# Optimization experiments

Measured on AMD Instinct MI355X. Metric: run time of the kernel, lower is better.

Reference implementation:

```python
import jax, jax.numpy as jnp
import numpy as np

N_NODES = 50000
N_EDGES = 800000
NODE_DIM = 32
EDGE_DIM = 16
HID = 64
MSG_HID = 128
NUM_GRAPHS = 512
NUM_MP = 3
S2S_STEPS = 6


def _lin(k, fan_in, fan_out):
    # torch Linear default init: U(-1/sqrt(fan_in), 1/sqrt(fan_in))
    bound = 1.0 / np.sqrt(fan_in)
    kw, kb = jax.random.split(k)
    W = jax.random.uniform(kw, (fan_in, fan_out), jnp.float32, -bound, bound)
    b = jax.random.uniform(kb, (fan_out,), jnp.float32, -bound, bound)
    return W, b


def setup_inputs() -> dict:
    key = jax.random.key(0)
    ks = jax.random.split(key, 16)
    x_feat = jax.random.normal(ks[0], (N_NODES, NODE_DIM), jnp.float32)
    edge_index = jax.random.randint(ks[1], (2, N_EDGES), 0, N_NODES)
    edge_attr = jax.random.normal(ks[2], (N_EDGES, EDGE_DIM), jnp.float32)
    batch = jnp.sort(jax.random.randint(ks[3], (N_NODES,), 0, NUM_GRAPHS))
    W_emb, b_emb = _lin(ks[4], NODE_DIM, HID)
    W_m1, b_m1 = _lin(ks[5], 2 * HID + EDGE_DIM, MSG_HID)
    W_m2, b_m2 = _lin(ks[6], MSG_HID, HID)
    bnd = 1.0 / np.sqrt(HID)
    gru_W_ih = jax.random.uniform(ks[7], (3 * HID, HID), jnp.float32, -bnd, bnd)
    gru_W_hh = jax.random.uniform(ks[8], (3 * HID, HID), jnp.float32, -bnd, bnd)
    gru_b_ih = jax.random.uniform(ks[9], (3 * HID,), jnp.float32, -bnd, bnd)
    gru_b_hh = jax.random.uniform(ks[9], (3 * HID,), jnp.float32, -bnd, bnd)
    lstm_W_ih = jax.random.uniform(ks[10], (4 * HID, 2 * HID), jnp.float32, -bnd, bnd)
    lstm_W_hh = jax.random.uniform(ks[11], (4 * HID, HID), jnp.float32, -bnd, bnd)
    lstm_b_ih = jax.random.uniform(ks[12], (4 * HID,), jnp.float32, -bnd, bnd)
    lstm_b_hh = jax.random.uniform(ks[12], (4 * HID,), jnp.float32, -bnd, bnd)
    W_r1, b_r1 = _lin(ks[13], 2 * HID, HID)
    W_r2, b_r2 = _lin(ks[14], HID, 1)
    return dict(x_feat=x_feat, edge_index=edge_index, edge_attr=edge_attr, batch=batch,
                W_emb=W_emb, b_emb=b_emb, W_m1=W_m1, b_m1=b_m1, W_m2=W_m2, b_m2=b_m2,
                gru_W_ih=gru_W_ih, gru_W_hh=gru_W_hh, gru_b_ih=gru_b_ih, gru_b_hh=gru_b_hh,
                lstm_W_ih=lstm_W_ih, lstm_W_hh=lstm_W_hh, lstm_b_ih=lstm_b_ih, lstm_b_hh=lstm_b_hh,
                W_r1=W_r1, b_r1=b_r1, W_r2=W_r2, b_r2=b_r2)


def reference(x_feat, edge_index, edge_attr, batch,
              W_emb, b_emb, W_m1, b_m1, W_m2, b_m2,
              gru_W_ih, gru_W_hh, gru_b_ih, gru_b_hh,
              lstm_W_ih, lstm_W_hh, lstm_b_ih, lstm_b_hh,
              W_r1, b_r1, W_r2, b_r2):
    src, dst = edge_index[0], edge_index[1]
    x = x_feat @ W_emb + b_emb  # [N, HID]
    h = x  # GRU hidden state (seq_len=1 GRU)
    for _ in range(NUM_MP):
        # message: cat([x_i (target), x_j (source), edge_attr]) -> MLP -> scatter-add to target
        mi = jnp.concatenate([x[dst], x[src], edge_attr], axis=-1)  # [E, 2H+Ed]
        msg = jnp.maximum(mi @ W_m1 + b_m1, 0.0) @ W_m2 + b_m2  # [E, H]
        m = jax.ops.segment_sum(msg, dst, num_segments=N_NODES)  # [N, H]
        # torch GRU cell, gate order (r, z, n)
        gi = m @ gru_W_ih.T + gru_b_ih
        gh = h @ gru_W_hh.T + gru_b_hh
        ir, iz, i_n = jnp.split(gi, 3, axis=-1)
        hr, hz, h_n = jnp.split(gh, 3, axis=-1)
        r = jax.nn.sigmoid(ir + hr)
        z = jax.nn.sigmoid(iz + hz)
        n = jnp.tanh(i_n + r * h_n)
        h = (1.0 - z) * n + z * h
        x = h
    # Set2Set pooling
    qh = jnp.zeros((NUM_GRAPHS, HID), x.dtype)
    qc = jnp.zeros((NUM_GRAPHS, HID), x.dtype)
    q_star = jnp.zeros((NUM_GRAPHS, 2 * HID), x.dtype)
    for _ in range(S2S_STEPS):
        # torch LSTM cell, gate order (i, f, g, o)
        g = q_star @ lstm_W_ih.T + lstm_b_ih + qh @ lstm_W_hh.T + lstm_b_hh
        gi_, gf, gg, go = jnp.split(g, 4, axis=-1)
        qc = jax.nn.sigmoid(gf) * qc + jax.nn.sigmoid(gi_) * jnp.tanh(gg)
        qh = jax.nn.sigmoid(go) * jnp.tanh(qc)
        e = jnp.sum(x * qh[batch], axis=-1)  # [N]
        emax = jax.ops.segment_max(e, batch, num_segments=NUM_GRAPHS)
        a = jnp.exp(e - emax[batch])
        asum = jax.ops.segment_sum(a, batch, num_segments=NUM_GRAPHS)
        a = a / asum[batch]  # segment softmax
        rvec = jax.ops.segment_sum(a[:, None] * x, batch, num_segments=NUM_GRAPHS)  # [B, H]
        q_star = jnp.concatenate([qh, rvec], axis=-1)
    out = jnp.maximum(q_star @ W_r1 + b_r1, 0.0) @ W_r2 + b_r2
    return out
```

## Files before the change

kernel.cpp:

```cpp
#include <hip/hip_runtime.h>
#include <hip/hip_bf16.h>

#define HID 64
#define MSG 128
#define NDIM 32
#define EDIM 16
#define NG 512
#define SCAP 192

typedef unsigned short u16;
typedef unsigned int u32;
typedef _Float16 h8 __attribute__((ext_vector_type(8)));
typedef _Float16 h4 __attribute__((ext_vector_type(4)));
typedef _Float16 h2 __attribute__((ext_vector_type(2)));

__device__ __forceinline__ float sigm(float x){return 1.0f/(1.0f+expf(-x));}
__device__ __forceinline__ int rfl(int x){return __builtin_amdgcn_readfirstlane(x);}
__device__ __forceinline__ u32 pkh(float a, float b){
    union { h2 h; u32 u; } v; v.h[0] = (_Float16)a; v.h[1] = (_Float16)b; return v.u;
}
__device__ __forceinline__ h2 pk2h(float a, float b){
    union { __fp16 __attribute__((ext_vector_type(2))) r; h2 h; } v;
    v.r = __builtin_amdgcn_cvt_pkrtz(a, b);
    return v.h;
}
__device__ __forceinline__ float fdot2_(h2 a, u32 w, float c){
    union { u32 u; h2 h; } v; v.u = w;
    return __builtin_amdgcn_fdot2(a, v.h, c, false);
}

__global__ void k_hist(const int* __restrict__ idx, int n, int* __restrict__ cnt) {
    int i = blockIdx.x * blockDim.x + threadIdx.x;
    int stride = gridDim.x * blockDim.x;
    for (; i < n; i += stride) atomicAdd(&cnt[idx[i]], 1);
}

__global__ void k_scanA(const int* __restrict__ in, int* __restrict__ out,
                        int* __restrict__ bsum, int n) {
    __shared__ int sh[1024];
    int i = blockIdx.x * 1024 + threadIdx.x;
    int v = (i < n) ? in[i] : 0;
    sh[threadIdx.x] = v;
    __syncthreads();
    for (int off = 1; off < 1024; off <<= 1) {
        int t = (threadIdx.x >= off) ? sh[threadIdx.x - off] : 0;
        __syncthreads();
        sh[threadIdx.x] += t;
        __syncthreads();
    }
    if (i < n) out[i] = sh[threadIdx.x] - v;
    if (threadIdx.x == 1023) bsum[blockIdx.x] = sh[1023];
}
__global__ void k_scanB(const int* __restrict__ bsum, int* __restrict__ boff, int nb) {
    if (threadIdx.x == 0) {
        int r = 0;
        for (int b = 0; b < nb; b++) { boff[b] = r; r += bsum[b]; }
        boff[nb] = r;
    }
}
__global__ void k_scanC(int* __restrict__ out, const int* __restrict__ boff, int n, int nb) {
    int i = blockIdx.x * blockDim.x + threadIdx.x;
    if (i < n) out[i] += boff[i >> 10];
    else if (i == n) out[n] = boff[nb];
}

__global__ void k_gptr(const int* __restrict__ batch, int N, int* __restrict__ gptr) {
    int g = blockIdx.x * blockDim.x + threadIdx.x;
    if (g > NG) return;
    int lo = 0, hi = N;
    while (lo < hi) { int mid = (lo + hi) >> 1; if (batch[mid] < g) lo = mid + 1; else hi = mid; }
    gptr[g] = lo;
}

__global__ void k_scatter(const int* __restrict__ src, const int* __restrict__ dst, int n,
                          const int* __restrict__ ptr, int* __restrict__ cursor,
                          int* __restrict__ eidx, int* __restrict__ slist) {
    int i = blockIdx.x * blockDim.x + threadIdx.x;
    int stride = gridDim.x * blockDim.x;
    for (; i < n; i += stride) {
        int d = dst[i];
        int pos = ptr[d] + atomicAdd(&cursor[d], 1);
        eidx[pos] = i;
        slist[pos] = src[i];
    }
}

__global__ void k_permea(const int* __restrict__ eidx, const float* __restrict__ ea,
                         _Float16* __restrict__ eap, int E) {
    int i = blockIdx.x * blockDim.x + threadIdx.x;
    if (i >= E) return;
    int e = eidx[i];
    const float* s = ea + (size_t)e * EDIM;
    float4 a = *(const float4*)s, b = *(const float4*)(s + 4);
    float4 c = *(const float4*)(s + 8), d = *(const float4*)(s + 12);
    h8 o0, o1;
    o0[0]=(_Float16)a.x; o0[1]=(_Float16)a.y; o0[2]=(_Float16)a.z; o0[3]=(_Float16)a.w;
    o0[4]=(_Float16)b.x; o0[5]=(_Float16)b.y; o0[6]=(_Float16)b.z; o0[7]=(_Float16)b.w;
    o1[0]=(_Float16)c.x; o1[1]=(_Float16)c.y; o1[2]=(_Float16)c.z; o1[3]=(_Float16)c.w;
    o1[4]=(_Float16)d.x; o1[5]=(_Float16)d.y; o1[6]=(_Float16)d.z; o1[7]=(_Float16)d.w;
    h8* dp = (h8*)(eap + (size_t)i * EDIM);
    dp[0] = o0; dp[1] = o1;
}

__global__ void k_fuse(const float* __restrict__ Wih, const float* __restrict__ Whh,
                       const float* __restrict__ W2, const float* __restrict__ bm2,
                       uint4* __restrict__ gGA, uint2* __restrict__ gGB,
                       uint4* __restrict__ gUA, uint2* __restrict__ gUB,
                       float* __restrict__ gbb) {
    int t = blockIdx.x * blockDim.x + threadIdx.x;
    if (t < 2048) {
        int k4 = t >> 6, c = t & 63;
        float G[3][4];
#pragma unroll
        for (int g = 0; g < 3; g++)
#pragma unroll
            for (int kk = 0; kk < 4; kk++) {
                int j = 4 * k4 + kk;
                const float* w2r = W2 + (size_t)j * 64;
                const float* wir = Wih + (size_t)(g * 64 + c) * 64;
                float s = 0.f;
                for (int k = 0; k < 64; k++) s += w2r[k] * wir[k];
                G[g][kk] = s;
            }
        uint4 A; uint2 B;
        A.x = pkh(G[0][0], G[0][1]); A.y = pkh(G[1][0], G[1][1]);
        A.z = pkh(G[2][0], G[2][1]); A.w = pkh(G[0][2], G[0][3]);
        B.x = pkh(G[1][2], G[1][3]); B.y = pkh(G[2][2], G[2][3]);
        gGA[t] = A; gGB[t] = B;
    } else if (t < 3072) {
        int u = t - 2048;
        int k4 = u >> 6, c = u & 63;
        float U[3][4];
#pragma unroll
        for (int g = 0; g < 3; g++)
#pragma unroll
            for (int kk = 0; kk < 4; kk++)
                U[g][kk] = Whh[(size_t)(g * 64 + c) * 64 + 4 * k4 + kk];
        uint4 A; uint2 B;
        A.x = pkh(U[0][0], U[0][1]); A.y = pkh(U[1][0], U[1][1]);
        A.z = pkh(U[2][0], U[2][1]); A.w = pkh(U[0][2], U[0][3]);
        B.x = pkh(U[1][2], U[1][3]); B.y = pkh(U[2][2], U[2][3]);
        gUA[u] = A; gUB[u] = B;
    } else if (t < 3072 + 192) {
        int cg = t - 3072;
        const float* wir = Wih + (size_t)cg * 64;
        float s = 0.f;
        for (int k = 0; k < 64; k++) s += bm2[k] * wir[k];
        gbb[cg] = s;
    }
}

__global__ void k_packl(const float* __restrict__ lWih, const float* __restrict__ lWhh,
                        float* __restrict__ WT1, float* __restrict__ WT2) {
    int t = blockIdx.x * blockDim.x + threadIdx.x;
    if (t < 256 * 128) { int g = t >> 7, k = t & 127; WT1[k * 256 + g] = lWih[g * 128 + k]; }
    if (t < 256 * 64)  { int g = t >> 6, k = t & 63;  WT2[k * 256 + g] = lWhh[g * 64 + k]; }
}

__global__ void k_embed(const float* __restrict__ xf, const float* __restrict__ We,
                        const float* __restrict__ be, float* __restrict__ xh, int N) {
    __shared__ float Wl[NDIM * HID];
    for (int t = threadIdx.x; t < NDIM * HID; t += blockDim.x) Wl[t] = We[t];
    __syncthreads();
    int total = N * HID;
    int stride = gridDim.x * blockDim.x;
    for (int idx = blockIdx.x * blockDim.x + threadIdx.x; idx < total; idx += stride) {
        int n = idx >> 6, c = idx & 63;
        const float* xr = xf + n * NDIM;
        float acc = be[c];
#pragma unroll
        for (int k = 0; k < NDIM; k++) acc += xr[k] * Wl[k * HID + c];
        xh[idx] = acc;
    }
}

__global__ void __launch_bounds__(256)
k_prep(const float* __restrict__ xh, const float* __restrict__ Wm1,
       const float* __restrict__ bm1, float* __restrict__ Hb,
       _Float16* __restrict__ PsH, int N) {
    __shared__ float Wl[64 * 256];
    for (int t = threadIdx.x; t < 64 * 256; t += 256) {
        int k = t >> 8, cc = t & 255;
        Wl[t] = (cc < 128) ? Wm1[k * 128 + cc] : Wm1[(64 + k) * 128 + (cc - 128)];
    }
    __syncthreads();
    int wv = threadIdx.x >> 6, lane = threadIdx.x & 63;
    int cc = lane * 4;
    float4 bias;
    if (lane < 32) bias = *(const float4*)&bm1[cc];
    else bias = make_float4(0.f, 0.f, 0.f, 0.f);
    int ngroups = (N + 7) >> 3;
    for (int g = blockIdx.x * 4 + wv; g < ngroups; g += gridDim.x * 4) {
        int base = rfl(g) * 8;
        const float* xp[8];
#pragma unroll
        for (int t = 0; t < 8; t++) {
            int d = base + t; if (d > N - 1) d = N - 1;
            xp[t] = xh + (size_t)d * 64;
        }
        float4 acc[8];
#pragma unroll
        for (int t = 0; t < 8; t++) acc[t] = bias;
#pragma unroll 2
        for (int k4 = 0; k4 < 16; k4++) {
            int k = k4 * 4;
            float4 xv4[8];
#pragma unroll
            for (int t = 0; t < 8; t++) xv4[t] = *(const float4*)&xp[t][k];
#pragma unroll
            for (int kk = 0; kk < 4; kk++) {
                float4 w = *(const float4*)&Wl[(k + kk) * 256 + cc];
#pragma unroll
                for (int t = 0; t < 8; t++) {
                    float xv = kk == 0 ? xv4[t].x : kk == 1 ? xv4[t].y : kk == 2 ? xv4[t].z : xv4[t].w;
                    acc[t].x += xv * w.x; acc[t].y += xv * w.y;
                    acc[t].z += xv * w.z; acc[t].w += xv * w.w;
                }
            }
        }
#pragma unroll
        for (int t = 0; t < 8; t++) {
            int d = base + t;
            if (d < N) {
                if (lane < 32) *(float4*)&Hb[(size_t)d * 128 + cc] = acc[t];
                else {
                    h4 o;
                    o[0] = (_Float16)acc[t].x; o[1] = (_Float16)acc[t].y;
                    o[2] = (_Float16)acc[t].z; o[3] = (_Float16)acc[t].w;
                    *(h4*)&PsH[(size_t)d * 128 + (cc - 128)] = o;
                }
            }
        }
    }
}

__global__ void __launch_bounds__(256)
k_edge(const _Float16* __restrict__ PsH, const _Float16* __restrict__ eap,
       const float* __restrict__ Wm1, const int* __restrict__ ptr,
       const int* __restrict__ slist, float* __restrict__ Hb, int N) {
    int c = threadIdx.x & 127;
    int half = threadIdx.x >> 7;
    h2 wh[8];
#pragma unroll
    for (int k = 0; k < 8; k++) {
        h2 t;
        t[0] = (_Float16)Wm1[128 * 128 + (2 * k) * 128 + c];
        t[1] = (_Float16)Wm1[128 * 128 + (2 * k + 1) * 128 + c];
        wh[k] = t;
    }
    for (int dd = blockIdx.x * 2 + half; dd < N; dd += gridDim.x * 2) {
        int d = rfl(dd);
        float pd = Hb[(size_t)d * 128 + c];
        int eb = rfl(ptr[d]), ee = rfl(ptr[d + 1]);
        const int* sp = slist + eb;
        const _Float16* ep = eap + (size_t)eb * EDIM;
        int ne = ee - eb;
        float acc = 0.f;
        int i = 0;
        for (; i + 8 <= ne; i += 8) {
            int ns[8];
#pragma unroll
            for (int j = 0; j < 8; j++) ns[j] = rfl(sp[i + j]);
            float pv[8];
#pragma unroll
            for (int j = 0; j < 8; j++) pv[j] = (float)PsH[(size_t)ns[j] * 128 + c];
#pragma unroll
            for (int j = 0; j < 8; j++) {
                union { uint4 u; h2 h[4]; } A, B;
                A.u = *(const uint4*)(ep + (size_t)(i + j) * EDIM);
                B.u = *(const uint4*)(ep + (size_t)(i + j) * EDIM + 8);
                float pe = 0.f;
#pragma unroll
                for (int k = 0; k < 4; k++) pe = __builtin_amdgcn_fdot2(A.h[k], wh[k], pe, false);
#pragma unroll
                for (int k = 0; k < 4; k++) pe = __builtin_amdgcn_fdot2(B.h[k], wh[4 + k], pe, false);
                acc += fmaxf(pd + pv[j] + pe, 0.f);
            }
        }
        for (; i < ne; i++) {
            int n0 = rfl(sp[i]);
            float pv = (float)PsH[(size_t)n0 * 128 + c];
            union { uint4 u; h2 h[4]; } A, B;
            A.u = *(const uint4*)(ep + (size_t)i * EDIM);
            B.u = *(const uint4*)(ep + (size_t)i * EDIM + 8);
            float pe = 0.f;
#pragma unroll
            for (int k = 0; k < 4; k++) pe = __builtin_amdgcn_fdot2(A.h[k], wh[k], pe, false);
#pragma unroll
            for (int k = 0; k < 4; k++) pe = __builtin_amdgcn_fdot2(B.h[k], wh[4 + k], pe, false);
            acc += fmaxf(pd + pv + pe, 0.f);
        }
        Hb[(size_t)d * 128 + c] = acc;
    }
}

__global__ void __launch_bounds__(256)
k_node(const float* __restrict__ H, const uint4* __restrict__ gGA, const uint2* __restrict__ gGB,
       const uint4* __restrict__ gUA, const uint2* __restrict__ gUB,
       const float* __restrict__ gbb, const float* __restrict__ bih, const float* __restrict__ bhh,
       const int* __restrict__ ptr, const float* __restrict__ xin, float* __restrict__ xout, int N) {
    extern __shared__ char smem[];
    uint4* GA = (uint4*)smem;
    uint2* GB = (uint2*)(smem + 32768);
    uint4* UA = (uint4*)(smem + 49152);
    uint2* UB = (uint2*)(smem + 65536);
    for (int t = threadIdx.x; t < 2048; t += 256) { GA[t] = gGA[t]; GB[t] = gGB[t]; }
    for (int t = threadIdx.x; t < 1024; t += 256) { UA[t] = gUA[t]; UB[t] = gUB[t]; }
    __syncthreads();
    int wv = threadIdx.x >> 6, lane = threadIdx.x & 63;
    float gbr = gbb[lane], gbz = gbb[64 + lane], gbn = gbb[128 + lane];
    float br = bih[lane], bz = bih[64 + lane], bn = bih[128 + lane];
    float cr = bhh[lane], cz = bhh[64 + lane], cn = bhh[128 + lane];
    for (int dd = blockIdx.x * 4 + wv; dd < N; dd += gridDim.x * 4) {
        int d = rfl(dd);
        const float* hp = H + (size_t)d * 128;
        const float* xp = xin + (size_t)d * 64;
        float hv = xp[lane];
        float deg = (float)(ptr[d + 1] - ptr[d]);
        float gr = br + deg * gbr, gz = bz + deg * gbz, gn = bn + deg * gbn;
#pragma unroll 2
        for (int k4 = 0; k4 < 32; k4++) {
            float4 hx = *(const float4*)&hp[k4 * 4];
            h2 a01 = pk2h(hx.x, hx.y), a23 = pk2h(hx.z, hx.w);
            uint4 wa = GA[k4 * 64 + lane];
            uint2 wb = GB[k4 * 64 + lane];
            gr = fdot2_(a01, wa.x, gr); gz = fdot2_(a01, wa.y, gz); gn = fdot2_(a01, wa.z, gn);
            gr = fdot2_(a23, wa.w, gr); gz = fdot2_(a23, wb.x, gz); gn = fdot2_(a23, wb.y, gn);
        }
        float hr_ = cr, hz_ = cz, hn_ = cn;
#pragma unroll 2
        for (int k4 = 0; k4 < 16; k4++) {
            float4 hx = *(const float4*)&xp[k4 * 4];
            h2 a01 = pk2h(hx.x, hx.y), a23 = pk2h(hx.z, hx.w);
            uint4 wa = UA[k4 * 64 + lane];
            uint2 wb = UB[k4 * 64 + lane];
            hr_ = fdot2_(a01, wa.x, hr_); hz_ = fdot2_(a01, wa.y, hz_); hn_ = fdot2_(a01, wa.z, hn_);
            hr_ = fdot2_(a23, wa.w, hr_); hz_ = fdot2_(a23, wb.x, hz_); hn_ = fdot2_(a23, wb.y, hn_);
        }
        float r = sigm(gr + hr_);
        float z = sigm(gz + hz_);
        float nn = tanhf(gn + r * hn_);
        xout[(size_t)d * 64 + lane] = (1.f - z) * nn + z * hv;
    }
}

__global__ void __launch_bounds__(1024)
k_s2s(const float* __restrict__ xh, const int* __restrict__ gptr,
      const float* __restrict__ WT1, const float* __restrict__ WT2,
      const float* __restrict__ lbih, const float* __restrict__ lbhh,
      const float* __restrict__ Wr1, const float* __restrict__ br1,
      const float* __restrict__ Wr2, const float* __restrict__ br2,
      float* __restrict__ out) {
    int b = blockIdx.x, tid = threadIdx.x;
    __shared__ float xl[SCAP * 64];
    __shared__ float qs[128], qhl[64], qcs[64], g[256], red[16], asums[16], rvs[1024];
    int start = gptr[b], end = gptr[b + 1];
    int seg = end - start;
    bool uselds = (seg <= SCAP);
    if (uselds) {
        int tot = seg * 64;
        for (int t = tid; t < tot; t += 1024) xl[t] = xh[(size_t)start * 64 + t];
    }
    if (tid < 128) qs[tid] = 0.f;
    if (tid < 64) { qhl[tid] = 0.f; qcs[tid] = 0.f; }
    __syncthreads();
    int grp = tid >> 6, lane = tid & 63;
    int gate = tid & 255, part = tid >> 8;
    for (int s = 0; s < 6; s++) {
        {
            float acc = 0.f;
            int k0 = part * 32;
#pragma unroll 8
            for (int k = k0; k < k0 + 32; k++) acc += qs[k] * WT1[k * 256 + gate];
            int k1 = part * 16;
#pragma unroll 8
            for (int k = k1; k < k1 + 16; k++) acc += qhl[k] * WT2[k * 256 + gate];
            rvs[tid] = acc;
        }
        __syncthreads();
        if (tid < 256) g[tid] = lbih[tid] + lbhh[tid] + rvs[tid] + rvs[256 + tid] + rvs[512 + tid] + rvs[768 + tid];
        __syncthreads();
        if (tid < 64) {
            float ig = sigm(g[tid]), fg = sigm(g[64 + tid]);
            float gg = tanhf(g[128 + tid]), og = sigm(g[192 + tid]);
            float c = fg * qcs[tid] + ig * gg;
            float h = og * tanhf(c);
            qcs[tid] = c; qhl[tid] = h; qs[tid] = h;
        }
        __syncthreads();
        float qv = qhl[lane];
        float mloc = -3.4e38f, asl = 0.f, rv = 0.f;
        for (int n = grp; n < seg; n += 16) {
            float xv = uselds ? xl[n * 64 + lane] : xh[(size_t)(start + n) * 64 + lane];
            float p = xv * qv;
#pragma unroll
            for (int off = 32; off > 0; off >>= 1) p += __shfl_xor(p, off);
            float mnew = fmaxf(mloc, p);
            float corr = expf(mloc - mnew);
            float a = expf(p - mnew);
            asl = asl * corr + a;
            rv = rv * corr + a * xv;
            mloc = mnew;
        }
        if (lane == 0) red[grp] = mloc;
        __syncthreads();
        float gmax = red[0];
#pragma unroll
        for (int j = 1; j < 16; j++) gmax = fmaxf(gmax, red[j]);
        float sc = expf(mloc - gmax);
        rvs[tid] = rv * sc;
        if (lane == 0) asums[grp] = asl * sc;
        __syncthreads();
        if (tid < 64) {
            float rt = 0.f, at = 0.f;
#pragma unroll
            for (int j = 0; j < 16; j++) { rt += rvs[tid + 64 * j]; at += asums[j]; }
            qs[64 + tid] = (at > 0.f) ? rt / at : 0.f;
        }
        __syncthreads();
    }
    if (tid < 64) {
        float a2 = br1[tid];
#pragma unroll 8
        for (int k = 0; k < 128; k++) a2 += qs[k] * Wr1[k * 64 + tid];
        a2 = fmaxf(a2, 0.f);
        float v = a2 * Wr2[tid];
#pragma unroll
        for (int off = 32; off > 0; off >>= 1) v += __shfl_xor(v, off);
        if (tid == 0) out[b] = v + br2[0];
    }
}

extern "C" void kernel_launch(void* const* d_in, const int* in_sizes, int n_in,
                              void* d_out, int out_size, void* d_ws, size_t ws_size,
                              hipStream_t stream) {
    const float* x_feat = (const float*)d_in[0];
    const int*   ei     = (const int*)d_in[1];
    const float* eattr  = (const float*)d_in[2];
    const int*   batch  = (const int*)d_in[3];
    const float* W_emb  = (const float*)d_in[4];
    const float* b_emb  = (const float*)d_in[5];
    const float* W_m1   = (const float*)d_in[6];
    const float* b_m1   = (const float*)d_in[7];
    const float* W_m2   = (const float*)d_in[8];
    const float* b_m2   = (const float*)d_in[9];
    const float* gWih   = (const float*)d_in[10];
    const float* gWhh   = (const float*)d_in[11];
    const float* gbih   = (const float*)d_in[12];
    const float* gbhh   = (const float*)d_in[13];
    const float* lWih   = (const float*)d_in[14];
    const float* lWhh   = (const float*)d_in[15];
    const float* lbih   = (const float*)d_in[16];
    const float* lbhh   = (const float*)d_in[17];
    const float* Wr1    = (const float*)d_in[18];
    const float* br1    = (const float*)d_in[19];
    const float* Wr2    = (const float*)d_in[20];
    const float* br2    = (const float*)d_in[21];

    int N = in_sizes[0] / NDIM;
    int E = in_sizes[1] / 2;

    char* w = (char*)d_ws;
    auto alloc = [&](size_t b) { char* p = w; w += (b + 511) & ~(size_t)511; return p; };
    float*     xh    = (float*)alloc((size_t)N * 64 * 4);
    float*     xh2   = (float*)alloc((size_t)N * 64 * 4);
    _Float16*  PsH   = (_Float16*)alloc((size_t)N * 128 * 2);
    float*     Hb    = (float*)alloc((size_t)N * 128 * 4);
    int*       ptr   = (int*)alloc((size_t)(N + 1) * 4);
    int*       slist = (int*)alloc((size_t)E * 4);
    int*       eidx  = (int*)alloc((size_t)E * 4);
    _Float16*  eap   = (_Float16*)alloc((size_t)E * EDIM * 2);
    uint4*     gGA   = (uint4*)alloc((size_t)2048 * 16);
    uint2*     gGB   = (uint2*)alloc((size_t)2048 * 8);
    uint4*     gUA   = (uint4*)alloc((size_t)1024 * 16);
    uint2*     gUB   = (uint2*)alloc((size_t)1024 * 8);
    float*     gbb   = (float*)alloc((size_t)192 * 4);
    float*     WT1   = (float*)alloc((size_t)128 * 256 * 4);
    float*     WT2   = (float*)alloc((size_t)64 * 256 * 4);
    int*       gptr  = (int*)alloc((size_t)(NG + 1) * 4);
    int*       bsum  = (int*)alloc(128 * 4);
    int*       boff  = (int*)alloc(128 * 4);
    char* z0 = w;
    int*       cnt    = (int*)alloc((size_t)N * 4);
    int*       cursor = (int*)alloc((size_t)N * 4);
    char* z0e = w;

    hipMemsetAsync(z0, 0, (size_t)(z0e - z0), stream);

    hipError_t attr_err = hipFuncSetAttribute((const void*)k_node,
        hipFuncAttributeMaxDynamicSharedMemorySize, 73728);
    (void)attr_err;

    int NB = (N + 1023) / 1024;
    k_hist<<<1024, 256, 0, stream>>>(ei + E, E, cnt);
    k_scanA<<<NB, 1024, 0, stream>>>(cnt, ptr, bsum, N);
    k_scanB<<<1, 64, 0, stream>>>(bsum, boff, NB);
    k_scanC<<<(N + 256) / 256, 256, 0, stream>>>(ptr, boff, N, NB);
    k_gptr<<<3, 256, 0, stream>>>(batch, N, gptr);
    k_scatter<<<3125, 256, 0, stream>>>(ei, ei + E, E, ptr, cursor, eidx, slist);
    k_permea<<<(E + 255) / 256, 256, 0, stream>>>(eidx, eattr, eap, E);
    k_fuse<<<13, 256, 0, stream>>>(gWih, gWhh, W_m2, b_m2, gGA, gGB, gUA, gUB, gbb);
    k_packl<<<128, 256, 0, stream>>>(lWih, lWhh, WT1, WT2);

    k_embed<<<2048, 256, 0, stream>>>(x_feat, W_emb, b_emb, xh, N);

    float* xa = xh;
    float* xb = xh2;
    for (int r = 0; r < 3; r++) {
        k_prep<<<391, 256, 0, stream>>>(xa, W_m1, b_m1, Hb, PsH, N);
        k_edge<<<4096, 256, 0, stream>>>(PsH, eap, W_m1, ptr, slist, Hb, N);
        k_node<<<512, 256, 73728, stream>>>(Hb, gGA, gGB, gUA, gUB, gbb, gbih, gbhh,
                                            ptr, xa, xb, N);
        float* t = xa; xa = xb; xb = t;
    }
    k_s2s<<<NG, 1024, 0, stream>>>(xa, gptr, WT1, WT2, lbih, lbhh,
                                   Wr1, br1, Wr2, br2, (float*)d_out);
}
```

Measured before the change: 1.071 ms.

## Fuse edge-attr permute into scatter and batch four nodes per wave in GRU

The edge scatter kernel now converts each edge's attributes to fp16 and writes them straight to their sorted position, which removes the separate permute kernel and the eidx buffer. The GRU node kernel now has each wave handle four nodes at once, so every LDS weight load is reused across four nodes instead of one. The cost is higher register pressure from four sets of accumulators, which may lower occupancy. The fused scatter also writes eap in scattered rather than contiguous order.

New measurement: 947.8 us. 1.13x faster.

```diff
diff --git a/kernel.cpp b/kernel.cpp
--- a/kernel.cpp
+++ b/kernel.cpp
@@ -72,34 +72,27 @@
     gptr[g] = lo;
 }
 
-__global__ void k_scatter(const int* __restrict__ src, const int* __restrict__ dst, int n,
+__global__ void k_scatter(const int* __restrict__ src, const int* __restrict__ dst,
+                          const float* __restrict__ ea, int n,
                           const int* __restrict__ ptr, int* __restrict__ cursor,
-                          int* __restrict__ eidx, int* __restrict__ slist) {
+                          int* __restrict__ slist, _Float16* __restrict__ eap) {
     int i = blockIdx.x * blockDim.x + threadIdx.x;
     int stride = gridDim.x * blockDim.x;
     for (; i < n; i += stride) {
         int d = dst[i];
         int pos = ptr[d] + atomicAdd(&cursor[d], 1);
-        eidx[pos] = i;
         slist[pos] = src[i];
-    }
-}
-
-__global__ void k_permea(const int* __restrict__ eidx, const float* __restrict__ ea,
-                         _Float16* __restrict__ eap, int E) {
-    int i = blockIdx.x * blockDim.x + threadIdx.x;
-    if (i >= E) return;
-    int e = eidx[i];
-    const float* s = ea + (size_t)e * EDIM;
-    float4 a = *(const float4*)s, b = *(const float4*)(s + 4);
-    float4 c = *(const float4*)(s + 8), d = *(const float4*)(s + 12);
-    h8 o0, o1;
-    o0[0]=(_Float16)a.x; o0[1]=(_Float16)a.y; o0[2]=(_Float16)a.z; o0[3]=(_Float16)a.w;
-    o0[4]=(_Float16)b.x; o0[5]=(_Float16)b.y; o0[6]=(_Float16)b.z; o0[7]=(_Float16)b.w;
-    o1[0]=(_Float16)c.x; o1[1]=(_Float16)c.y; o1[2]=(_Float16)c.z; o1[3]=(_Float16)c.w;
-    o1[4]=(_Float16)d.x; o1[5]=(_Float16)d.y; o1[6]=(_Float16)d.z; o1[7]=(_Float16)d.w;
-    h8* dp = (h8*)(eap + (size_t)i * EDIM);
-    dp[0] = o0; dp[1] = o1;
+        const float* s = ea + (size_t)i * EDIM;
+        float4 a = *(const float4*)s, b = *(const float4*)(s + 4);
+        float4 c = *(const float4*)(s + 8), d4 = *(const float4*)(s + 12);
+        h8 o0, o1;
+        o0[0]=(_Float16)a.x; o0[1]=(_Float16)a.y; o0[2]=(_Float16)a.z; o0[3]=(_Float16)a.w;
+        o0[4]=(_Float16)b.x; o0[5]=(_Float16)b.y; o0[6]=(_Float16)b.z; o0[7]=(_Float16)b.w;
+        o1[0]=(_Float16)c.x; o1[1]=(_Float16)c.y; o1[2]=(_Float16)c.z; o1[3]=(_Float16)c.w;
+        o1[4]=(_Float16)d4.x; o1[5]=(_Float16)d4.y; o1[6]=(_Float16)d4.z; o1[7]=(_Float16)d4.w;
+        h8* dp = (h8*)(eap + (size_t)pos * EDIM);
+        dp[0] = o0; dp[1] = o1;
+    }
 }
 
 __global__ void k_fuse(const float* __restrict__ Wih, const float* __restrict__ Whh,
@@ -311,36 +304,65 @@
     float gbr = gbb[lane], gbz = gbb[64 + lane], gbn = gbb[128 + lane];
     float br = bih[lane], bz = bih[64 + lane], bn = bih[128 + lane];
     float cr = bhh[lane], cz = bhh[64 + lane], cn = bhh[128 + lane];
-    for (int dd = blockIdx.x * 4 + wv; dd < N; dd += gridDim.x * 4) {
-        int d = rfl(dd);
-        const float* hp = H + (size_t)d * 128;
-        const float* xp = xin + (size_t)d * 64;
-        float hv = xp[lane];
-        float deg = (float)(ptr[d + 1] - ptr[d]);
-        float gr = br + deg * gbr, gz = bz + deg * gbz, gn = bn + deg * gbn;
+    int ngroups = (N + 3) >> 2;
+    for (int g = blockIdx.x * 4 + wv; g < ngroups; g += gridDim.x * 4) {
+        int base = rfl(g) * 4;
+        const float* hp[4]; const float* xp[4]; float deg[4];
+#pragma unroll
+        for (int t = 0; t < 4; t++) {
+            int d = base + t; if (d > N - 1) d = N - 1;
+            hp[t] = H + (size_t)d * 128;
+            xp[t] = xin + (size_t)d * 64;
+            deg[t] = (float)(ptr[d + 1] - ptr[d]);
+        }
+        float gr[4], gz[4], gn[4];
+#pragma unroll
+        for (int t = 0; t < 4; t++) {
+            gr[t] = br + deg[t] * gbr;
+            gz[t] = bz + deg[t] * gbz;
+            gn[t] = bn + deg[t] * gbn;
+        }
 #pragma unroll 2
         for (int k4 = 0; k4 < 32; k4++) {
-            float4 hx = *(const float4*)&hp[k4 * 4];
-            h2 a01 = pk2h(hx.x, hx.y), a23 = pk2h(hx.z, hx.w);
             uint4 wa = GA[k4 * 64 + lane];
             uint2 wb = GB[k4 * 64 + lane];
-            gr = fdot2_(a01, wa.x, gr); gz = fdot2_(a01, wa.y, gz); gn = fdot2_(a01, wa.z, gn);
-            gr = fdot2_(a23, wa.w, gr); gz = fdot2_(a23, wb.x, gz); gn = fdot2_(a23, wb.y, gn);
-        }
-        float hr_ = cr, hz_ = cz, hn_ = cn;
+#pragma unroll
+            for (int t = 0; t < 4; t++) {
+                float4 hx = *(const float4*)&hp[t][k4 * 4];
+                h2 a01 = pk2h(hx.x, hx.y), a23 = pk2h(hx.z, hx.w);
+                gr[t] = fdot2_(a01, wa.x, gr[t]); gz[t] = fdot2_(a01, wa.y, gz[t]);
+                gn[t] = fdot2_(a01, wa.z, gn[t]);
+                gr[t] = fdot2_(a23, wa.w, gr[t]); gz[t] = fdot2_(a23, wb.x, gz[t]);
+                gn[t] = fdot2_(a23, wb.y, gn[t]);
+            }
+        }
+        float hr[4], hz[4], hn[4], hv[4];
+#pragma unroll
+        for (int t = 0; t < 4; t++) { hr[t] = cr; hz[t] = cz; hn[t] = cn; hv[t] = xp[t][lane]; }
 #pragma unroll 2
         for (int k4 = 0; k4 < 16; k4++) {
-            float4 hx = *(const float4*)&xp[k4 * 4];
-            h2 a01 = pk2h(hx.x, hx.y), a23 = pk2h(hx.z, hx.w);
             uint4 wa = UA[k4 * 64 + lane];
             uint2 wb = UB[k4 * 64 + lane];
-            hr_ = fdot2_(a01, wa.x, hr_); hz_ = fdot2_(a01, wa.y, hz_); hn_ = fdot2_(a01, wa.z, hn_);
-            hr_ = fdot2_(a23, wa.w, hr_); hz_ = fdot2_(a23, wb.x, hz_); hn_ = fdot2_(a23, wb.y, hn_);
-        }
-        float r = sigm(gr + hr_);
-        float z = sigm(gz + hz_);
-        float nn = tanhf(gn + r * hn_);
-        xout[(size_t)d * 64 + lane] = (1.f - z) * nn + z * hv;
+#pragma unroll
+            for (int t = 0; t < 4; t++) {
+                float4 hx = *(const float4*)&xp[t][k4 * 4];
+                h2 a01 = pk2h(hx.x, hx.y), a23 = pk2h(hx.z, hx.w);
+                hr[t] = fdot2_(a01, wa.x, hr[t]); hz[t] = fdot2_(a01, wa.y, hz[t]);
+                hn[t] = fdot2_(a01, wa.z, hn[t]);
+                hr[t] = fdot2_(a23, wa.w, hr[t]); hz[t] = fdot2_(a23, wb.x, hz[t]);
+                hn[t] = fdot2_(a23, wb.y, hn[t]);
+            }
+        }
+#pragma unroll
+        for (int t = 0; t < 4; t++) {
+            int d = base + t;
+            if (d < N) {
+                float r = sigm(gr[t] + hr[t]);
+                float z = sigm(gz[t] + hz[t]);
+                float nn = tanhf(gn[t] + r * hn[t]);
+                xout[(size_t)d * 64 + lane] = (1.f - z) * nn + z * hv[t];
+            }
+        }
     }
 }
 
@@ -468,7 +490,6 @@
     float*     Hb    = (float*)alloc((size_t)N * 128 * 4);
     int*       ptr   = (int*)alloc((size_t)(N + 1) * 4);
     int*       slist = (int*)alloc((size_t)E * 4);
-    int*       eidx  = (int*)alloc((size_t)E * 4);
     _Float16*  eap   = (_Float16*)alloc((size_t)E * EDIM * 2);
     uint4*     gGA   = (uint4*)alloc((size_t)2048 * 16);
     uint2*     gGB   = (uint2*)alloc((size_t)2048 * 8);
@@ -497,8 +518,7 @@
     k_scanB<<<1, 64, 0, stream>>>(bsum, boff, NB);
     k_scanC<<<(N + 256) / 256, 256, 0, stream>>>(ptr, boff, N, NB);
     k_gptr<<<3, 256, 0, stream>>>(batch, N, gptr);
-    k_scatter<<<3125, 256, 0, stream>>>(ei, ei + E, E, ptr, cursor, eidx, slist);
-    k_permea<<<(E + 255) / 256, 256, 0, stream>>>(eidx, eattr, eap, E);
+    k_scatter<<<3125, 256, 0, stream>>>(ei, ei + E, eattr, E, ptr, cursor, slist, eap);
     k_fuse<<<13, 256, 0, stream>>>(gWih, gWhh, W_m2, b_m2, gGA, gGB, gUA, gUB, gbb);
     k_packl<<<128, 256, 0, stream>>>(lWih, lWhh, WT1, WT2);
 
```
